# Performance work log

Measured on AMD Instinct MI355X. Metric: run time of the kernel, lower is better.

The kernel has to match this reference:

```python
import jax, jax.numpy as jnp
import numpy as np

RES = 32
HEADS = 16
EMB = 1024
DIM_HEAD = EMB // HEADS
BATCH = 8
N = RES * RES
SCALE = DIM_HEAD ** -0.5


def _make_bias_idxs():
    # replicate the LeViT-style |dx|,|dy| offset indexing from __init__
    points = [(i, j) for i in range(RES) for j in range(RES)]
    offsets = {}
    idxs = []
    for p1 in points:
        for p2 in points:
            off = (abs(p1[0] - p2[0]), abs(p1[1] - p2[1]))
            if off not in offsets:
                offsets[off] = len(offsets)
            idxs.append(offsets[off])
    return np.asarray(idxs, dtype=np.int32).reshape(N, N), len(offsets)


def setup_inputs() -> dict:
    key = jax.random.key(0)
    k_x, k_qkv, k_b, k_o = jax.random.split(key, 4)
    bias_idxs, n_off = _make_bias_idxs()  # n_off == 1024 for a 32x32 grid
    return {
        "x": jax.random.normal(k_x, (BATCH, N, EMB), dtype=jnp.float32),
        "W_qkv": jax.random.normal(k_qkv, (3 * EMB, EMB), dtype=jnp.float32) * 0.02,
        "attention_biases": jax.random.normal(k_b, (HEADS, n_off), dtype=jnp.float32) * 0.02,
        "bias_idxs": jnp.asarray(bias_idxs),
        "W_out": jax.random.normal(k_o, (EMB, EMB), dtype=jnp.float32) * 0.02,
        "b_out": jnp.zeros((EMB,), dtype=jnp.float32),
    }


def reference(x, W_qkv, attention_biases, bias_idxs, W_out, b_out):
    B, n, E = x.shape
    # to_qkv: Linear(E, 3E, bias=False) -> x @ W^T
    qkv = x @ W_qkv.T  # [B, n, 3E]
    q, k, v = jnp.split(qkv, 3, axis=-1)

    def heads(t):  # b n (h d) -> b h n d
        return t.reshape(B, n, HEADS, DIM_HEAD).transpose(0, 2, 1, 3)

    q, k, v = heads(q), heads(k), heads(v)
    qk = jnp.einsum("bhnd,bhmd->bhnm", q, k) * SCALE  # [B, h, n, n]
    bias = attention_biases[:, bias_idxs]  # gather -> [h, n, n]
    qk = qk + bias[None]
    attn = jax.nn.softmax(qk, axis=-1)
    out = jnp.einsum("bhnm,bhmd->bhnd", attn, v)
    out = out.transpose(0, 2, 1, 3).reshape(B, n, E)  # b h n d -> b n (h d)
    # to_out: Linear(E, E) with bias (dropout p=0 is identity)
    return out @ W_out.T + b_out
```

## Files before the change

kernel.cpp:

```cpp
#include <hip/hip_runtime.h>

typedef __attribute__((ext_vector_type(8))) short bf16x8;
typedef __attribute__((ext_vector_type(4))) short bf16x4;
typedef __attribute__((ext_vector_type(4))) float f32x4;

#define L2E 1.44269504088896340736f
#define QSCL 0.18033688011112042f

__device__ inline unsigned short f2bf(float f) {
  union { float f; unsigned int u; } x; x.f = f;
  return (unsigned short)((x.u + 0x8000u) >> 16);
}
__device__ inline unsigned int f2bf2(float a, float b) {
  union { float f; unsigned int u; } xa, xb;
  xa.f = a; xb.f = b;
  return ((xa.u + 0x8000u) >> 16) | (((xb.u + 0x8000u) & 0xFFFF0000u));
}

__device__ inline void gl_lds16(const void* g, void* l) {
  __builtin_amdgcn_global_load_lds((const __attribute__((address_space(1))) void*)g,
                                   (__attribute__((address_space(3))) void*)l,
                                   16, 0, 0);
}

__device__ inline void vm_drain() {
  asm volatile("s_waitcnt vmcnt(0)" ::: "memory");
}

__global__ void cast_bf16_kernel(const float* __restrict__ in,
                                 unsigned short* __restrict__ out, int n4) {
  int i = blockIdx.x * blockDim.x + threadIdx.x;
  int st = gridDim.x * blockDim.x;
  for (; i < n4; i += st) {
    float4 v = reinterpret_cast<const float4*>(in)[i];
    ushort4 o;
    o.x = f2bf(v.x); o.y = f2bf(v.y); o.z = f2bf(v.z); o.w = f2bf(v.w);
    reinterpret_cast<ushort4*>(out)[i] = o;
  }
}

template <int MODE>
__global__ __launch_bounds__(256, 4) void gemm_qkv_t(
    const unsigned short* __restrict__ A,
    const unsigned short* __restrict__ Bm,
    unsigned short* __restrict__ qo,
    unsigned short* __restrict__ ko,
    unsigned short* __restrict__ vo) {
  __shared__ unsigned short sA[2][128 * 32];
  __shared__ unsigned short sB[2][128 * 32];
  const int K = 1024;
  const int tid = threadIdx.x;
  const int w = tid >> 6, lane = tid & 63;
  const int l15 = lane & 15, quad = lane >> 4;
  const int wm = (w >> 1) * 64, wn = (w & 1) * 64;
  const int tm = blockIdx.y;
  const int tn = (MODE == 0) ? blockIdx.x : blockIdx.x + 16;

  const unsigned short* Ab = A + (size_t)(tm * 128) * K;
  const unsigned short* Bb = Bm + (size_t)(tn * 128) * K;

  const int srow = w * 32 + (lane >> 2);
  const int scol = (((lane & 3) ^ ((lane >> 3) & 3))) * 8;
  const int rsw = (l15 >> 1) & 3;

  const f32x4 fz = {0.f, 0.f, 0.f, 0.f};
  f32x4 acc[4][4];
#pragma unroll
  for (int i = 0; i < 4; i++)
#pragma unroll
    for (int j = 0; j < 4; j++) acc[i][j] = fz;

  gl_lds16(Ab + (size_t)srow * K + scol,        &sA[0][(w * 32) * 32]);
  gl_lds16(Ab + (size_t)(srow + 16) * K + scol, &sA[0][(w * 32 + 16) * 32]);
  gl_lds16(Bb + (size_t)srow * K + scol,        &sB[0][(w * 32) * 32]);
  gl_lds16(Bb + (size_t)(srow + 16) * K + scol, &sB[0][(w * 32 + 16) * 32]);

  int buf = 0;
  for (int k0 = 0; k0 < K; k0 += 32) {
    vm_drain();
    __syncthreads();
    if (k0 + 32 < K) {
      int nb = buf ^ 1, kn = k0 + 32;
      gl_lds16(Ab + (size_t)srow * K + kn + scol,        &sA[nb][(w * 32) * 32]);
      gl_lds16(Ab + (size_t)(srow + 16) * K + kn + scol, &sA[nb][(w * 32 + 16) * 32]);
      gl_lds16(Bb + (size_t)srow * K + kn + scol,        &sB[nb][(w * 32) * 32]);
      gl_lds16(Bb + (size_t)(srow + 16) * K + kn + scol, &sB[nb][(w * 32 + 16) * 32]);
    }
    bf16x8 af[4], bfr[4];
#pragma unroll
    for (int mt = 0; mt < 4; mt++)
      af[mt] = *(const bf16x8*)&sA[buf][(wm + mt * 16 + l15) * 32 + ((quad ^ rsw) << 3)];
#pragma unroll
    for (int nt = 0; nt < 4; nt++)
      bfr[nt] = *(const bf16x8*)&sB[buf][(wn + nt * 16 + l15) * 32 + ((quad ^ rsw) << 3)];
#pragma unroll
    for (int mt = 0; mt < 4; mt++)
#pragma unroll
      for (int nt = 0; nt < 4; nt++) {
        if (MODE == 0)
          acc[mt][nt] = __builtin_amdgcn_mfma_f32_16x16x32_bf16(bfr[nt], af[mt], acc[mt][nt], 0, 0, 0);
        else
          acc[mt][nt] = __builtin_amdgcn_mfma_f32_16x16x32_bf16(af[mt], bfr[nt], acc[mt][nt], 0, 0, 0);
      }
    buf ^= 1;
  }

  const int m0 = tm * 128;
  const int bb = m0 >> 10, n0 = m0 & 1023;
  const int cbase = (tn * 128) & 1023;

  if (MODE == 0) {
    const int which = tn >> 3;
    const float scl = (which == 0) ? QSCL : 1.0f;
    unsigned short* dst = (which == 0) ? qo : ko;
#pragma unroll
    for (int mt = 0; mt < 4; mt++) {
      int tok = n0 + wm + mt * 16 + l15;
#pragma unroll
      for (int nt = 0; nt < 4; nt++) {
        int c = cbase + wn + nt * 16 + quad * 4;
        int hh = c >> 6, d0 = c & 63;
        uint2 val;
        val.x = f2bf2(acc[mt][nt][0] * scl, acc[mt][nt][1] * scl);
        val.y = f2bf2(acc[mt][nt][2] * scl, acc[mt][nt][3] * scl);
        *(uint2*)&dst[(((size_t)bb * 16 + hh) * 1024 + tok) * 64 + d0] = val;
      }
    }
  } else {
#pragma unroll
    for (int mt = 0; mt < 4; mt++) {
      int tok = n0 + wm + mt * 16 + quad * 4;
#pragma unroll
      for (int nt = 0; nt < 4; nt++) {
        int c = cbase + wn + nt * 16 + l15;
        int hh = c >> 6, dd = c & 63;
        uint2 val;
        val.x = f2bf2(acc[mt][nt][0], acc[mt][nt][1]);
        val.y = f2bf2(acc[mt][nt][2], acc[mt][nt][3]);
        *(uint2*)&vo[(((size_t)bb * 16 + hh) * 64 + dd) * 1024 + tok] = val;
      }
    }
  }
}

__global__ __launch_bounds__(256, 4) void attn_kernel(
    const unsigned short* __restrict__ Q,
    const unsigned short* __restrict__ Kg,
    const unsigned short* __restrict__ Vt,
    const float* __restrict__ biases,
    unsigned short* __restrict__ Og) {
  __shared__ unsigned short sK[2][64 * 64];
  __shared__ unsigned short sV[2][64 * 64];
  __shared__ float sBias[1024];

  const int bx = blockIdx.x;
  const int bh = bx & 127, qt = bx >> 7;
  const int h = bh & 15, b = bh >> 4;
  const int tid = threadIdx.x, w = tid >> 6, lane = tid & 63;
  const int l15 = lane & 15, quad = lane >> 4;

  const size_t bhs = (size_t)(b * 16 + h);
  const unsigned short* qbase = Q + (bhs * 1024 + (size_t)qt * 128) * 64;
  const unsigned short* kbase = Kg + bhs * 1024 * 64;
  const unsigned short* vbase = Vt + bhs * 64 * 1024;

  for (int t = tid; t < 1024; t += 256) sBias[t] = biases[h * 1024 + t] * L2E;

  const int sr0 = w * 16 + (lane >> 3);
  const int sc8 = lane & 7;
  const int sw0 = sc8 ^ (lane >> 3);

  gl_lds16(kbase + (size_t)sr0 * 64 + sw0 * 8,        &sK[0][(w * 16) * 64]);
  gl_lds16(kbase + (size_t)(sr0 + 8) * 64 + sw0 * 8,  &sK[0][(w * 16 + 8) * 64]);
  gl_lds16(vbase + (size_t)sr0 * 1024 + sw0 * 8,      &sV[0][(w * 16) * 64]);
  gl_lds16(vbase + (size_t)(sr0 + 8) * 1024 + sw0 * 8,&sV[0][(w * 16 + 8) * 64]);

  bf16x8 qf[2][2];
#pragma unroll
  for (int qb = 0; qb < 2; qb++)
#pragma unroll
    for (int kd = 0; kd < 2; kd++)
      qf[qb][kd] = *(const bf16x8*)(qbase + (w * 32 + qb * 16 + l15) * 64 + kd * 32 + quad * 8);

  const int qg0 = qt * 128 + w * 32;
  int qi[2], qj[2];
#pragma unroll
  for (int qb = 0; qb < 2; qb++) {
    int qr = qg0 + qb * 16 + l15;
    qi[qb] = qr >> 5; qj[qb] = qr & 31;
  }
  const int kvq = quad * 4;

  float rsum[2] = {0.f, 0.f};
  const f32x4 fz = {0.f, 0.f, 0.f, 0.f};
  f32x4 of[2][4];
#pragma unroll
  for (int i = 0; i < 2; i++)
#pragma unroll
    for (int j = 0; j < 4; j++) of[i][j] = fz;

  int buf = 0;
  for (int j0 = 0; j0 < 1024; j0 += 64) {
    vm_drain();
    __syncthreads();
    if (j0 + 64 < 1024) {
      int nb = buf ^ 1, jn = j0 + 64;
      gl_lds16(kbase + (size_t)(jn + sr0) * 64 + sw0 * 8,       &sK[nb][(w * 16) * 64]);
      gl_lds16(kbase + (size_t)(jn + sr0 + 8) * 64 + sw0 * 8,   &sK[nb][(w * 16 + 8) * 64]);
      gl_lds16(vbase + (size_t)sr0 * 1024 + jn + sw0 * 8,       &sV[nb][(w * 16) * 64]);
      gl_lds16(vbase + (size_t)(sr0 + 8) * 1024 + jn + sw0 * 8, &sV[nb][(w * 16 + 8) * 64]);
    }
    const unsigned short* K_ = sK[buf];
    const unsigned short* V_ = sV[buf];
    const int j5 = j0 >> 5;

#pragma unroll
    for (int kvb = 0; kvb < 4; kvb++) {
      bf16x8 kf0 = *(const bf16x8*)&K_[(kvb * 16 + l15) * 64 + ((quad ^ (l15 & 7)) << 3)];
      bf16x8 kf1 = *(const bf16x8*)&K_[(kvb * 16 + l15) * 64 + (((4 + quad) ^ (l15 & 7)) << 3)];
      bf16x4 vf[4];
#pragma unroll
      for (int nt = 0; nt < 4; nt++) {
        int d = nt * 16 + l15;
        vf[nt] = *(const bf16x4*)&V_[d * 64 + (((kvb * 2 + (quad >> 1)) ^ (l15 & 7)) << 3) + (quad & 1) * 4];
      }
      const int kvi = j5 + (kvb >> 1);
      const int kvjb = (kvb & 1) * 16 + kvq;
#pragma unroll
      for (int qb = 0; qb < 2; qb++) {
        f32x4 s4 = __builtin_amdgcn_mfma_f32_16x16x32_bf16(kf0, qf[qb][0], fz, 0, 0, 0);
        s4 = __builtin_amdgcn_mfma_f32_16x16x32_bf16(kf1, qf[qb][1], s4, 0, 0, 0);
        const float* bb = sBias + (abs(qi[qb] - kvi) << 5);
        float p0 = __builtin_amdgcn_exp2f(s4.x + bb[abs(qj[qb] - kvjb)]);
        float p1 = __builtin_amdgcn_exp2f(s4.y + bb[abs(qj[qb] - (kvjb + 1))]);
        float p2 = __builtin_amdgcn_exp2f(s4.z + bb[abs(qj[qb] - (kvjb + 2))]);
        float p3 = __builtin_amdgcn_exp2f(s4.w + bb[abs(qj[qb] - (kvjb + 3))]);
        rsum[qb] += (p0 + p1) + (p2 + p3);
        union { unsigned int u[2]; bf16x4 v; } pk;
        pk.u[0] = f2bf2(p0, p1);
        pk.u[1] = f2bf2(p2, p3);
#pragma unroll
        for (int nt = 0; nt < 4; nt++)
          of[qb][nt] = __builtin_amdgcn_mfma_f32_16x16x16bf16_1k(pk.v, vf[nt], of[qb][nt], 0, 0, 0);
      }
    }
    buf ^= 1;
  }

#pragma unroll
  for (int qb = 0; qb < 2; qb++) {
    rsum[qb] += __shfl_xor(rsum[qb], 16);
    rsum[qb] += __shfl_xor(rsum[qb], 32);
  }

#pragma unroll
  for (int qb = 0; qb < 2; qb++)
#pragma unroll
    for (int r = 0; r < 4; r++) {
      float rv = __shfl(rsum[qb], kvq + r, 16);
      float inv = __builtin_amdgcn_rcpf(rv);
      int n = qg0 + qb * 16 + kvq + r;
      size_t orow = ((size_t)b * 1024 + n) * 1024 + h * 64;
#pragma unroll
      for (int nt = 0; nt < 4; nt++)
        Og[orow + nt * 16 + l15] = f2bf(of[qb][nt][r] * inv);
    }
}

__global__ __launch_bounds__(256, 4) void gemm_out_k(
    const unsigned short* __restrict__ A,
    const unsigned short* __restrict__ Bm,
    const float* __restrict__ bias,
    float* __restrict__ out) {
  __shared__ unsigned short sA[2][128 * 32];
  __shared__ unsigned short sB[2][128 * 32];
  const int K = 1024;
  const int tid = threadIdx.x;
  const int w = tid >> 6, lane = tid & 63;
  const int l15 = lane & 15, quad = lane >> 4;
  const int wm = (w >> 1) * 64, wn = (w & 1) * 64;
  const int tm = blockIdx.y, tn = blockIdx.x;

  const unsigned short* Ab = A + (size_t)(tm * 128) * K;
  const unsigned short* Bb = Bm + (size_t)(tn * 128) * K;

  const int srow = w * 32 + (lane >> 2);
  const int scol = (((lane & 3) ^ ((lane >> 3) & 3))) * 8;
  const int rsw = (l15 >> 1) & 3;

  const f32x4 fz = {0.f, 0.f, 0.f, 0.f};
  f32x4 acc[4][4];
#pragma unroll
  for (int i = 0; i < 4; i++)
#pragma unroll
    for (int j = 0; j < 4; j++) acc[i][j] = fz;

  gl_lds16(Ab + (size_t)srow * K + scol,        &sA[0][(w * 32) * 32]);
  gl_lds16(Ab + (size_t)(srow + 16) * K + scol, &sA[0][(w * 32 + 16) * 32]);
  gl_lds16(Bb + (size_t)srow * K + scol,        &sB[0][(w * 32) * 32]);
  gl_lds16(Bb + (size_t)(srow + 16) * K + scol, &sB[0][(w * 32 + 16) * 32]);

  int buf = 0;
  for (int k0 = 0; k0 < K; k0 += 32) {
    vm_drain();
    __syncthreads();
    if (k0 + 32 < K) {
      int nb = buf ^ 1, kn = k0 + 32;
      gl_lds16(Ab + (size_t)srow * K + kn + scol,        &sA[nb][(w * 32) * 32]);
      gl_lds16(Ab + (size_t)(srow + 16) * K + kn + scol, &sA[nb][(w * 32 + 16) * 32]);
      gl_lds16(Bb + (size_t)srow * K + kn + scol,        &sB[nb][(w * 32) * 32]);
      gl_lds16(Bb + (size_t)(srow + 16) * K + kn + scol, &sB[nb][(w * 32 + 16) * 32]);
    }
    bf16x8 af[4], bfr[4];
#pragma unroll
    for (int mt = 0; mt < 4; mt++)
      af[mt] = *(const bf16x8*)&sA[buf][(wm + mt * 16 + l15) * 32 + ((quad ^ rsw) << 3)];
#pragma unroll
    for (int nt = 0; nt < 4; nt++)
      bfr[nt] = *(const bf16x8*)&sB[buf][(wn + nt * 16 + l15) * 32 + ((quad ^ rsw) << 3)];
#pragma unroll
    for (int mt = 0; mt < 4; mt++)
#pragma unroll
      for (int nt = 0; nt < 4; nt++)
        acc[mt][nt] = __builtin_amdgcn_mfma_f32_16x16x32_bf16(af[mt], bfr[nt], acc[mt][nt], 0, 0, 0);
    buf ^= 1;
  }

  const int m0 = tm * 128 + wm, c0 = tn * 128 + wn;
#pragma unroll
  for (int mt = 0; mt < 4; mt++)
#pragma unroll
    for (int nt = 0; nt < 4; nt++)
#pragma unroll
      for (int r = 0; r < 4; r++) {
        int m = m0 + mt * 16 + quad * 4 + r;
        int c = c0 + nt * 16 + l15;
        out[(size_t)m * 1024 + c] = acc[mt][nt][r] + bias[c];
      }
}

extern "C" void kernel_launch(void* const* d_in, const int* in_sizes, int n_in,
                              void* d_out, int out_size, void* d_ws, size_t ws_size,
                              hipStream_t stream) {
  const float* x    = (const float*)d_in[0];
  const float* Wqkv = (const float*)d_in[1];
  const float* ab   = (const float*)d_in[2];
  const float* Wout = (const float*)d_in[4];
  const float* bout = (const float*)d_in[5];
  float* out = (float*)d_out;

  char* ws = (char*)d_ws;
  unsigned short* xb  = (unsigned short*)(ws);
  unsigned short* wqb = (unsigned short*)(ws + 16777216);
  unsigned short* wob = (unsigned short*)(ws + 23068672);
  unsigned short* qw  = (unsigned short*)(ws + 25165824);
  unsigned short* kw  = (unsigned short*)(ws + 41943040);
  unsigned short* vw  = (unsigned short*)(ws + 58720256);
  unsigned short* ow  = (unsigned short*)(ws + 75497472);

  cast_bf16_kernel<<<1024, 256, 0, stream>>>(x, xb, 8192 * 1024 / 4);
  cast_bf16_kernel<<<512, 256, 0, stream>>>(Wqkv, wqb, 3072 * 1024 / 4);
  cast_bf16_kernel<<<256, 256, 0, stream>>>(Wout, wob, 1024 * 1024 / 4);
  gemm_qkv_t<0><<<dim3(16, 64), 256, 0, stream>>>(xb, wqb, qw, kw, vw);
  gemm_qkv_t<1><<<dim3(8, 64), 256, 0, stream>>>(xb, wqb, qw, kw, vw);
  attn_kernel<<<1024, 256, 0, stream>>>(qw, kw, vw, ab, ow);
  gemm_out_k<<<dim3(8, 64), 256, 0, stream>>>(ow, wob, bout, out);
}
```

Before: 274.6 us.

## Merge cast and QKV kernels, precompute bias offsets, compute row sums via MFMA

The three cast kernels become one launch, and the two QKV GEMM template launches become a single 24-column grid that branches at runtime on whether a tile belongs to Q/K or V. In attention, the per-element bias index math is replaced by precomputed column offsets and a wave-uniform row base per KV tile. Row sums now come from an extra MFMA against a ones vector instead of scalar adds plus shuffles. The goal is fewer launches and less VALU work in the softmax loop, at the cost of one extra MFMA per block and a runtime branch inside the GEMM.

```diff
diff --git a/kernel.cpp b/kernel.cpp
--- a/kernel.cpp
+++ b/kernel.cpp
@@ -27,20 +27,30 @@
   asm volatile("s_waitcnt vmcnt(0)" ::: "memory");
 }
 
-__global__ void cast_bf16_kernel(const float* __restrict__ in,
-                                 unsigned short* __restrict__ out, int n4) {
+#define N4_X  2097152
+#define N4_WQ 786432
+#define N4_WO 262144
+__global__ void cast3_kernel(const float* __restrict__ x,
+                             const float* __restrict__ wq,
+                             const float* __restrict__ wo,
+                             unsigned short* __restrict__ xb,
+                             unsigned short* __restrict__ wqb,
+                             unsigned short* __restrict__ wob) {
   int i = blockIdx.x * blockDim.x + threadIdx.x;
   int st = gridDim.x * blockDim.x;
-  for (; i < n4; i += st) {
-    float4 v = reinterpret_cast<const float4*>(in)[i];
+  for (; i < N4_X + N4_WQ + N4_WO; i += st) {
+    const float* src; unsigned short* dst; int j;
+    if (i < N4_X)            { src = x;  dst = xb;  j = i; }
+    else if (i < N4_X + N4_WQ){ src = wq; dst = wqb; j = i - N4_X; }
+    else                     { src = wo; dst = wob; j = i - N4_X - N4_WQ; }
+    float4 v = reinterpret_cast<const float4*>(src)[j];
     ushort4 o;
     o.x = f2bf(v.x); o.y = f2bf(v.y); o.z = f2bf(v.z); o.w = f2bf(v.w);
-    reinterpret_cast<ushort4*>(out)[i] = o;
-  }
-}
-
-template <int MODE>
-__global__ __launch_bounds__(256, 4) void gemm_qkv_t(
+    reinterpret_cast<ushort4*>(dst)[j] = o;
+  }
+}
+
+__global__ __launch_bounds__(256, 4) void gemm_qkv(
     const unsigned short* __restrict__ A,
     const unsigned short* __restrict__ Bm,
     unsigned short* __restrict__ qo,
@@ -53,8 +63,8 @@
   const int w = tid >> 6, lane = tid & 63;
   const int l15 = lane & 15, quad = lane >> 4;
   const int wm = (w >> 1) * 64, wn = (w & 1) * 64;
-  const int tm = blockIdx.y;
-  const int tn = (MODE == 0) ? blockIdx.x : blockIdx.x + 16;
+  const int tm = blockIdx.y, tn = blockIdx.x;
+  const bool qkmode = (tn < 16);
 
   const unsigned short* Ab = A + (size_t)(tm * 128) * K;
   const unsigned short* Bb = Bm + (size_t)(tn * 128) * K;
@@ -93,15 +103,19 @@
 #pragma unroll
     for (int nt = 0; nt < 4; nt++)
       bfr[nt] = *(const bf16x8*)&sB[buf][(wn + nt * 16 + l15) * 32 + ((quad ^ rsw) << 3)];
-#pragma unroll
-    for (int mt = 0; mt < 4; mt++)
-#pragma unroll
-      for (int nt = 0; nt < 4; nt++) {
-        if (MODE == 0)
+    if (qkmode) {
+#pragma unroll
+      for (int mt = 0; mt < 4; mt++)
+#pragma unroll
+        for (int nt = 0; nt < 4; nt++)
           acc[mt][nt] = __builtin_amdgcn_mfma_f32_16x16x32_bf16(bfr[nt], af[mt], acc[mt][nt], 0, 0, 0);
-        else
+    } else {
+#pragma unroll
+      for (int mt = 0; mt < 4; mt++)
+#pragma unroll
+        for (int nt = 0; nt < 4; nt++)
           acc[mt][nt] = __builtin_amdgcn_mfma_f32_16x16x32_bf16(af[mt], bfr[nt], acc[mt][nt], 0, 0, 0);
-      }
+    }
     buf ^= 1;
   }
 
@@ -109,7 +123,7 @@
   const int bb = m0 >> 10, n0 = m0 & 1023;
   const int cbase = (tn * 128) & 1023;
 
-  if (MODE == 0) {
+  if (qkmode) {
     const int which = tn >> 3;
     const float scl = (which == 0) ? QSCL : 1.0f;
     unsigned short* dst = (which == 0) ? qo : ko;
@@ -183,21 +197,25 @@
       qf[qb][kd] = *(const bf16x8*)(qbase + (w * 32 + qb * 16 + l15) * 64 + kd * 32 + quad * 8);
 
   const int qg0 = qt * 128 + w * 32;
-  int qi[2], qj[2];
-#pragma unroll
-  for (int qb = 0; qb < 2; qb++) {
-    int qr = qg0 + qb * 16 + l15;
-    qi[qb] = qr >> 5; qj[qb] = qr & 31;
-  }
-  const int kvq = quad * 4;
-
-  float rsum[2] = {0.f, 0.f};
+  const int qiw = __builtin_amdgcn_readfirstlane(qt * 4 + w);
+  int djo[2][2][4];
+#pragma unroll
+  for (int qb = 0; qb < 2; qb++)
+#pragma unroll
+    for (int kp = 0; kp < 2; kp++)
+#pragma unroll
+      for (int r = 0; r < 4; r++)
+        djo[qb][kp][r] = abs(qb * 16 + l15 - kp * 16 - quad * 4 - r);
+
   const f32x4 fz = {0.f, 0.f, 0.f, 0.f};
-  f32x4 of[2][4];
-#pragma unroll
-  for (int i = 0; i < 2; i++)
+  f32x4 of[2][4], osum[2];
+#pragma unroll
+  for (int i = 0; i < 2; i++) {
+    osum[i] = fz;
 #pragma unroll
     for (int j = 0; j < 4; j++) of[i][j] = fz;
+  }
+  const bf16x4 vones = {(short)0x3F80, (short)0x3F80, (short)0x3F80, (short)0x3F80};
 
   int buf = 0;
   for (int j0 = 0; j0 < 1024; j0 += 64) {
@@ -213,6 +231,9 @@
     const unsigned short* K_ = sK[buf];
     const unsigned short* V_ = sV[buf];
     const int j5 = j0 >> 5;
+    const int dh = qiw - j5;
+    const float* bA = sBias + (abs(dh) << 5);
+    const float* bB = sBias + (abs(dh - 1) << 5);
 
 #pragma unroll
     for (int kvb = 0; kvb < 4; kvb++) {
@@ -224,41 +245,34 @@
         int d = nt * 16 + l15;
         vf[nt] = *(const bf16x4*)&V_[d * 64 + (((kvb * 2 + (quad >> 1)) ^ (l15 & 7)) << 3) + (quad & 1) * 4];
       }
-      const int kvi = j5 + (kvb >> 1);
-      const int kvjb = (kvb & 1) * 16 + kvq;
+      const float* bp = (kvb < 2) ? bA : bB;
+      const int kp = kvb & 1;
 #pragma unroll
       for (int qb = 0; qb < 2; qb++) {
         f32x4 s4 = __builtin_amdgcn_mfma_f32_16x16x32_bf16(kf0, qf[qb][0], fz, 0, 0, 0);
         s4 = __builtin_amdgcn_mfma_f32_16x16x32_bf16(kf1, qf[qb][1], s4, 0, 0, 0);
-        const float* bb = sBias + (abs(qi[qb] - kvi) << 5);
-        float p0 = __builtin_amdgcn_exp2f(s4.x + bb[abs(qj[qb] - kvjb)]);
-        float p1 = __builtin_amdgcn_exp2f(s4.y + bb[abs(qj[qb] - (kvjb + 1))]);
-        float p2 = __builtin_amdgcn_exp2f(s4.z + bb[abs(qj[qb] - (kvjb + 2))]);
-        float p3 = __builtin_amdgcn_exp2f(s4.w + bb[abs(qj[qb] - (kvjb + 3))]);
-        rsum[qb] += (p0 + p1) + (p2 + p3);
+        float p0 = __builtin_amdgcn_exp2f(s4.x + bp[djo[qb][kp][0]]);
+        float p1 = __builtin_amdgcn_exp2f(s4.y + bp[djo[qb][kp][1]]);
+        float p2 = __builtin_amdgcn_exp2f(s4.z + bp[djo[qb][kp][2]]);
+        float p3 = __builtin_amdgcn_exp2f(s4.w + bp[djo[qb][kp][3]]);
         union { unsigned int u[2]; bf16x4 v; } pk;
         pk.u[0] = f2bf2(p0, p1);
         pk.u[1] = f2bf2(p2, p3);
 #pragma unroll
         for (int nt = 0; nt < 4; nt++)
           of[qb][nt] = __builtin_amdgcn_mfma_f32_16x16x16bf16_1k(pk.v, vf[nt], of[qb][nt], 0, 0, 0);
+        osum[qb] = __builtin_amdgcn_mfma_f32_16x16x16bf16_1k(pk.v, vones, osum[qb], 0, 0, 0);
       }
     }
     buf ^= 1;
   }
 
-#pragma unroll
-  for (int qb = 0; qb < 2; qb++) {
-    rsum[qb] += __shfl_xor(rsum[qb], 16);
-    rsum[qb] += __shfl_xor(rsum[qb], 32);
-  }
-
+  const int kvq = quad * 4;
 #pragma unroll
   for (int qb = 0; qb < 2; qb++)
 #pragma unroll
     for (int r = 0; r < 4; r++) {
-      float rv = __shfl(rsum[qb], kvq + r, 16);
-      float inv = __builtin_amdgcn_rcpf(rv);
+      float inv = __builtin_amdgcn_rcpf(osum[qb][r]);
       int n = qg0 + qb * 16 + kvq + r;
       size_t orow = ((size_t)b * 1024 + n) * 1024 + h * 64;
 #pragma unroll
@@ -358,11 +372,8 @@
   unsigned short* vw  = (unsigned short*)(ws + 58720256);
   unsigned short* ow  = (unsigned short*)(ws + 75497472);
 
-  cast_bf16_kernel<<<1024, 256, 0, stream>>>(x, xb, 8192 * 1024 / 4);
-  cast_bf16_kernel<<<512, 256, 0, stream>>>(Wqkv, wqb, 3072 * 1024 / 4);
-  cast_bf16_kernel<<<256, 256, 0, stream>>>(Wout, wob, 1024 * 1024 / 4);
-  gemm_qkv_t<0><<<dim3(16, 64), 256, 0, stream>>>(xb, wqb, qw, kw, vw);
-  gemm_qkv_t<1><<<dim3(8, 64), 256, 0, stream>>>(xb, wqb, qw, kw, vw);
+  cast3_kernel<<<1536, 256, 0, stream>>>(x, Wqkv, Wout, xb, wqb, wob);
+  gemm_qkv<<<dim3(24, 64), 256, 0, stream>>>(xb, wqb, qw, kw, vw);
   attn_kernel<<<1024, 256, 0, stream>>>(qw, kw, vw, ab, ow);
   gemm_out_k<<<dim3(8, 64), 256, 0, stream>>>(ow, wob, bout, out);
 }
```

New measurement: 927.2 us. 3.38x slower.
